# Kernel tuning notes

Hardware: AMD Instinct MI355X
Metric: run time of the kernel (lower is better)

## Reference

```python
import jax, jax.numpy as jnp
import numpy as np

NUM_RELATIONS = 3
NUM_HEADS = 1

N_NODES = 50000
N_EDGES = 300000
D = 256  # in_channels == out_channels == out_channels*num_heads
W_SCALE = 0.02  # realistic init scale; keeps linear-attention normalizer dominated by N_r


def setup_inputs() -> dict:
    key = jax.random.key(0)
    k = jax.random.split(key, 7)
    x = jax.random.normal(k[0], (N_NODES, D), dtype=jnp.float32)
    Wq = jax.random.normal(k[1], (NUM_RELATIONS, D, D * NUM_HEADS), dtype=jnp.float32) * W_SCALE
    Wk = jax.random.normal(k[2], (NUM_RELATIONS, D, D * NUM_HEADS), dtype=jnp.float32) * W_SCALE
    Wv = jax.random.normal(k[3], (NUM_RELATIONS, D, D * NUM_HEADS), dtype=jnp.float32) * W_SCALE
    Whp = jax.random.normal(k[4], (D * NUM_HEADS, D), dtype=jnp.float32) * W_SCALE
    edge_index = jax.random.randint(k[5], (2, N_EDGES), 0, N_NODES, dtype=jnp.int64)
    edge_type = jax.random.randint(k[6], (N_EDGES,), 0, NUM_RELATIONS, dtype=jnp.int64)
    return {"x": x, "Wq": Wq, "Wk": Wk, "Wv": Wv, "Whp": Whp,
            "edge_index": edge_index, "edge_type": edge_type}


def _trans_conv(x, Wq, Wk, Wv, Whp, edge_index, edge_type):
    # x: [N, F], Wq/Wk/Wv: [R, F, H*Dh], Whp: [H*Dh, Dh], edge_index: [2, E]
    row, col = edge_index[0], edge_index[1]
    N = x.shape[0]
    R = Wq.shape[0]
    H = NUM_HEADS
    Dh = Wq.shape[-1] // H
    xr = x[row]  # [E, F] gathered source-node features
    xc = x[col]  # [E, F] gathered target-node features
    x_out = jnp.zeros((N, Dh), dtype=x.dtype)
    for r in range(R):  # small fixed relation loop (structurally distinct weights)
        m = (edge_type == r).astype(x.dtype)  # [E] relation mask (handles ragged sizes)
        Nr = jnp.sum(m)  # number of edges of this relation (the 'N' in full_attention_conv)
        q = (xr @ Wq[r]).reshape(-1, H, Dh)  # [E, H, Dh]
        kk = (xc @ Wk[r]).reshape(-1, H, Dh)
        v = (xc @ Wv[r]).reshape(-1, H, Dh)
        # linear attention (no softmax), masked so only relation-r edges contribute
        kvs = jnp.einsum('e,ehm,ehd->hmd', m, kk, v)        # [H, Dh, Dh]
        num = jnp.einsum('ehm,hmd->ehd', q, kvs) + Nr * v    # [E, H, Dh]
        ks_sum = jnp.einsum('e,ehm->hm', m, kk)              # [H, Dh]
        norm = jnp.einsum('ehm,hm->eh', q, ks_sum)[..., None] + Nr  # [E, H, 1]
        attn = (num / norm).mean(axis=1)                     # [E, Dh] (mean over heads)
        x_out = x_out.at[row].add(m[:, None] * attn)         # scatter-add to source nodes
    return x_out @ Whp  # head projection


def reference(x, Wq, Wk, Wv, Whp, edge_index, edge_type):
    return _trans_conv(x, Wq, Wk, Wv, Whp, edge_index, edge_type)
```

## Files before the change

kernel.cpp:

```cpp
#include <hip/hip_runtime.h>

#define NN 50000
#define EE 300000
#define DD 256
#define RR 3
#define NPAD 50048
#define GS 64
#define SCT (RR * NN)
#define SCB 1024
#define SNB ((SCT + SCB - 1) / SCB)
#define TBLK 3128
#define WBLK 2560
#define CBLK 512
#define SBLK 12500

using bf16x8 = __attribute__((ext_vector_type(8))) short;
using f32x4  = __attribute__((ext_vector_type(4))) float;

__device__ __forceinline__ float bf2f(unsigned short u) {
    return __uint_as_float(((unsigned)u) << 16);
}
__device__ __forceinline__ unsigned short f2bf(float f) {
    unsigned u = __float_as_uint(f);
    return (unsigned short)((u + 0x7fffu + ((u >> 16) & 1u)) >> 16);
}
__device__ __forceinline__ void gload_lds16(const void* g, void* l) {
    __builtin_amdgcn_global_load_lds(
        (const __attribute__((address_space(1))) unsigned int*)g,
        (__attribute__((address_space(3))) unsigned int*)l, 16, 0, 0);
}

__global__ __launch_bounds__(256) void prep_tc(
    const float* __restrict__ x, const float* __restrict__ Wq,
    const float* __restrict__ Wk, const float* __restrict__ Wv,
    const float* __restrict__ Whp,
    unsigned short* __restrict__ xb, unsigned short* __restrict__ xT,
    unsigned short* __restrict__ Wqb, unsigned short* __restrict__ Wkb,
    unsigned short* __restrict__ Wvb, unsigned short* __restrict__ WhpT,
    const int* __restrict__ erow, const int* __restrict__ ecol,
    const int* __restrict__ etype, int* __restrict__ c_in,
    int* __restrict__ c_out, int* __restrict__ nr)
{
    const int tid = threadIdx.x;
    if (blockIdx.x < TBLK) {
        __shared__ unsigned short t[64][66];
        const int tb = blockIdx.x;
        const int n0 = (tb % 782) * 64, i0 = (tb / 782) * 64;
        const int nl = tid >> 2, c0 = (tid & 3) * 16;
        unsigned short vb[16];
        int n = n0 + nl;
        if (n < NN) {
            const float* src = x + (size_t)n * DD + i0 + c0;
#pragma unroll
            for (int q = 0; q < 16; q += 4) {
                float4 v = *(const float4*)(src + q);
                vb[q] = f2bf(v.x); vb[q + 1] = f2bf(v.y);
                vb[q + 2] = f2bf(v.z); vb[q + 3] = f2bf(v.w);
            }
#pragma unroll
            for (int q = 0; q < 16; q += 4)
                *(ushort4*)(xb + (size_t)n * DD + i0 + c0 + q) =
                    make_ushort4(vb[q], vb[q + 1], vb[q + 2], vb[q + 3]);
        } else {
#pragma unroll
            for (int q = 0; q < 16; q++) vb[q] = 0;
        }
#pragma unroll
        for (int q = 0; q < 16; q++) t[nl][c0 + q] = vb[q];
        __syncthreads();
        const int il = tid >> 2, nc0 = (tid & 3) * 16;
        unsigned short ob[16];
#pragma unroll
        for (int q = 0; q < 16; q++) ob[q] = t[nc0 + q][il];
#pragma unroll
        for (int q = 0; q < 16; q += 4)
            *(ushort4*)(xT + (size_t)(i0 + il) * NPAD + n0 + nc0 + q) =
                make_ushort4(ob[q], ob[q + 1], ob[q + 2], ob[q + 3]);
    } else if (blockIdx.x < TBLK + WBLK) {
        int t = (blockIdx.x - TBLK) * 256 + tid;
        int slot = t >> 16, o = t & 65535;
        int a = o >> 8, b = o & 255;
        if (slot < 3)       Wqb[(size_t)slot * 65536 + o] = f2bf(Wq[(size_t)slot * 65536 + o]);
        else if (slot < 6)  Wkb[(size_t)(slot - 3) * 65536 + o] = f2bf(Wk[(size_t)(slot - 3) * 65536 + o]);
        else if (slot < 9)  Wvb[(size_t)(slot - 6) * 65536 + o] = f2bf(Wv[(size_t)(slot - 6) * 65536 + o]);
        else if (slot == 9) WhpT[o] = f2bf(Whp[b * 256 + a]);
    } else {
        __shared__ int lnr[RR];
        if (tid < RR) lnr[tid] = 0;
        __syncthreads();
        int cb = blockIdx.x - (TBLK + WBLK);
        for (int e = cb * 256 + tid; e < EE; e += CBLK * 256) {
            int t = etype[e];
            atomicAdd(&c_out[t * NN + erow[e]], 1);
            atomicAdd(&c_in[t * NN + ecol[e]], 1);
            atomicAdd(&lnr[t], 1);
        }
        __syncthreads();
        if (tid < RR) atomicAdd(&nr[tid], lnr[tid]);
    }
}

__global__ __launch_bounds__(256) void prep2(
    const int* __restrict__ c_out, int* __restrict__ bsum,
    const unsigned short* __restrict__ xT, const int* __restrict__ c_in,
    float* __restrict__ xw, unsigned short* __restrict__ wbf)
{
    const int tid = threadIdx.x;
    if (blockIdx.x < SNB) {
        __shared__ int ws[4];
        const int b = blockIdx.x;
        const int i = b * SCB + tid * 4;
        int s = 0;
        if (i < SCT) {
            int4 v = *(const int4*)(c_out + i);
            s = v.x + v.y + v.z + v.w;
        }
#pragma unroll
        for (int off = 32; off; off >>= 1) s += __shfl_down(s, off, 64);
        if ((tid & 63) == 0) ws[tid >> 6] = s;
        __syncthreads();
        if (tid == 0) bsum[b] = ws[0] + ws[1] + ws[2] + ws[3];
    } else if (blockIdx.x < SNB + 256) {
        __shared__ float red[3][4];
        const int i = blockIdx.x - SNB;
        float a0 = 0.f, a1 = 0.f, a2 = 0.f;
        for (int n = tid * 4; n < NN; n += 1024) {
            ushort4 xv = *(const ushort4*)(xT + (size_t)i * NPAD + n);
            int4 w0 = *(const int4*)(c_in + n);
            int4 w1 = *(const int4*)(c_in + NN + n);
            int4 w2 = *(const int4*)(c_in + 2 * NN + n);
            float f0 = bf2f(xv.x), f1 = bf2f(xv.y), f2 = bf2f(xv.z), f3 = bf2f(xv.w);
            a0 += f0 * w0.x + f1 * w0.y + f2 * w0.z + f3 * w0.w;
            a1 += f0 * w1.x + f1 * w1.y + f2 * w1.z + f3 * w1.w;
            a2 += f0 * w2.x + f1 * w2.y + f2 * w2.z + f3 * w2.w;
        }
#pragma unroll
        for (int off = 32; off; off >>= 1) {
            a0 += __shfl_down(a0, off, 64);
            a1 += __shfl_down(a1, off, 64);
            a2 += __shfl_down(a2, off, 64);
        }
        if ((tid & 63) == 0) {
            red[0][tid >> 6] = a0; red[1][tid >> 6] = a1; red[2][tid >> 6] = a2;
        }
        __syncthreads();
        if (tid < 3)
            xw[tid * 256 + i] = red[tid][0] + red[tid][1] + red[tid][2] + red[tid][3];
    } else {
        int t = (blockIdx.x - SNB - 256) * 256 + tid;
        if (t < 3 * NPAD) {
            int r = t / NPAD, n = t % NPAD;
            wbf[t] = f2bf(n < NN ? (float)c_in[r * NN + n] : 0.f);
        }
    }
}

__global__ __launch_bounds__(256) void scan_bot(
    const int* __restrict__ cnt, const int* __restrict__ bsum,
    int* __restrict__ off, int* __restrict__ cur)
{
    __shared__ int bs[256], loc[256];
    const int b = blockIdx.x, tid = threadIdx.x;
    int v = tid < SNB ? bsum[tid] : 0;
    bs[tid] = v;
    __syncthreads();
    for (int d = 1; d < 256; d <<= 1) {
        int t = (tid >= d) ? bs[tid - d] : 0;
        __syncthreads();
        bs[tid] += t;
        __syncthreads();
    }
    const int myboff = b ? bs[b - 1] : 0;
    const int total = bs[255];
    const int i = b * SCB + tid * 4;
    int4 vv = make_int4(0, 0, 0, 0);
    if (i < SCT) vv = *(const int4*)(cnt + i);
    int s = vv.x + vv.y + vv.z + vv.w;
    loc[tid] = s;
    __syncthreads();
    for (int d = 1; d < 256; d <<= 1) {
        int t = (tid >= d) ? loc[tid - d] : 0;
        __syncthreads();
        loc[tid] += t;
        __syncthreads();
    }
    if (i < SCT) {
        int pre = myboff + (tid ? loc[tid - 1] : 0);
        int4 o;
        o.x = pre;
        o.y = pre + vv.x;
        o.z = pre + vv.x + vv.y;
        o.w = pre + vv.x + vv.y + vv.z;
        *(int4*)(off + i) = o;
        *(int4*)(cur + i) = o;
    }
    if (b == 0 && tid == 0) off[SCT] = total;
}

__global__ __launch_bounds__(256) void fill_kernel(
    const int* __restrict__ erow, const int* __restrict__ ecol,
    const int* __restrict__ etype, int* __restrict__ cur,
    int* __restrict__ scol)
{
    int e = blockIdx.x * 256 + threadIdx.x;
    if (e < EE) {
        int key = etype[e] * NN + erow[e];
        int p = atomicAdd(&cur[key], 1);
        scol[p] = ecol[e];
    }
}

__global__ __launch_bounds__(512) void g_kernel(
    const unsigned short* __restrict__ xT, const unsigned short* __restrict__ wbf,
    float* __restrict__ Gp)
{
    __shared__ __align__(16) char ldsA[16384];
    __shared__ __align__(16) char ldsB[16384];
    const int tid = threadIdx.x, lane = tid & 63, wid = tid >> 6;
    const int wr = wid >> 1, wc = wid & 1;
    const int i0 = blockIdx.x * 128, j0 = blockIdx.y * 128;
    const int TPZ = (NPAD / 64 + GS - 1) / GS;
    const int kt0 = blockIdx.z * TPZ;
    const int kt1 = min(NPAD / 64, kt0 + TPZ);

    f32x4 acc[3][2][4];
#pragma unroll
    for (int r = 0; r < 3; r++)
#pragma unroll
        for (int m = 0; m < 2; m++)
#pragma unroll
            for (int n = 0; n < 4; n++) acc[r][m][n] = (f32x4){0.f, 0.f, 0.f, 0.f};

    for (int kt = kt0; kt < kt1; kt++) {
        const int kbyte = kt * 128;
#pragma unroll
        for (int is = 0; is < 2; is++) {
            int lb = is * 8192 + wid * 1024;
            int d = lb + lane * 16;
            int row = d >> 7;
            int sc_ = (d & 127) ^ ((row & 7) << 4);
            gload_lds16((const char*)xT + (size_t)(i0 + row) * (NPAD * 2) + kbyte + sc_, ldsA + lb);
            gload_lds16((const char*)xT + (size_t)(j0 + row) * (NPAD * 2) + kbyte + sc_, ldsB + lb);
        }
        __syncthreads();
#pragma unroll
        for (int kk = 0; kk < 2; kk++) {
            const int cb = kk * 64 + ((lane >> 4) << 4);
            bf16x8 bfr[4];
#pragma unroll
            for (int n = 0; n < 4; n++) {
                int rn = wc * 64 + n * 16 + (lane & 15);
                bfr[n] = *(const bf16x8*)(ldsB + rn * 128 + (cb ^ ((rn & 7) << 4)));
            }
            float au[2][8];
#pragma unroll
            for (int m = 0; m < 2; m++) {
                int row = wr * 32 + m * 16 + (lane & 15);
                bf16x8 ar = *(const bf16x8*)(ldsA + row * 128 + (cb ^ ((row & 7) << 4)));
#pragma unroll
                for (int q = 0; q < 8; q++) au[m][q] = bf2f((unsigned short)ar[q]);
            }
            const int nb = kt * 64 + kk * 32 + ((lane >> 4) << 3);
#pragma unroll
            for (int r = 0; r < 3; r++) {
                bf16x8 wv = *(const bf16x8*)(wbf + (size_t)r * NPAD + nb);
                float wf[8];
#pragma unroll
                for (int q = 0; q < 8; q++) wf[q] = bf2f((unsigned short)wv[q]);
                bf16x8 am[2];
#pragma unroll
                for (int m = 0; m < 2; m++)
#pragma unroll
                    for (int q = 0; q < 8; q++)
                        am[m][q] = (short)f2bf(au[m][q] * wf[q]);
#pragma unroll
                for (int m = 0; m < 2; m++)
#pragma unroll
                    for (int n = 0; n < 4; n++)
                        acc[r][m][n] = __builtin_amdgcn_mfma_f32_16x16x32_bf16(
                            am[m], bfr[n], acc[r][m][n], 0, 0, 0);
            }
        }
        __syncthreads();
    }
    float* base = Gp + ((size_t)blockIdx.z * 4 + blockIdx.x * 2 + blockIdx.y) * 3 * 16384;
#pragma unroll
    for (int r = 0; r < 3; r++)
#pragma unroll
        for (int m = 0; m < 2; m++)
#pragma unroll
            for (int n = 0; n < 4; n++) {
                int col = wc * 64 + n * 16 + (lane & 15);
                int rw0 = wr * 32 + m * 16 + ((lane >> 4) << 2);
#pragma unroll
                for (int reg = 0; reg < 4; reg++)
                    base[r * 16384 + (rw0 + reg) * 128 + col] = acc[r][m][n][reg];
            }
}

__global__ __launch_bounds__(256) void greduce_kernel(
    const float* __restrict__ Gp, unsigned short* __restrict__ Gb)
{
    int gid = blockIdx.x * 256 + threadIdx.x;
    int t = gid >> 14, rem = gid & 16383;
    int r = t % 3, tile = t / 3;
    float s = 0.f;
    for (int z = 0; z < GS; z++)
        s += Gp[(size_t)z * 196608 + ((size_t)tile * 3 + r) * 16384 + rem];
    int i = (tile >> 1) * 128 + (rem >> 7);
    int j = (tile & 1) * 128 + (rem & 127);
    Gb[(size_t)r * 65536 + i * 256 + j] = f2bf(s);
}

__global__ __launch_bounds__(256) void matvec_bf(
    const unsigned short* __restrict__ Mat, const float* __restrict__ v,
    float* __restrict__ y)
{
    __shared__ float vs[256];
    const int b = blockIdx.x;
    const int r = b >> 6, rb = (b & 63) * 4;
    const int tid = threadIdx.x;
    vs[tid] = v[r * 256 + tid];
    __syncthreads();
    const int wid = tid >> 6, lane = tid & 63;
    const int row = rb + wid;
    ushort4 m4 = *(const ushort4*)(Mat + (size_t)r * 65536 + row * 256 + lane * 4);
    float s = bf2f(m4.x) * vs[lane * 4] + bf2f(m4.y) * vs[lane * 4 + 1] +
              bf2f(m4.z) * vs[lane * 4 + 2] + bf2f(m4.w) * vs[lane * 4 + 3];
#pragma unroll
    for (int off = 32; off; off >>= 1) s += __shfl_down(s, off, 64);
    if (lane == 0) y[r * 256 + row] = s;
}

__global__ __launch_bounds__(256) void sssum_kernel(
    const unsigned short* __restrict__ xb, const int* __restrict__ scol,
    const int* __restrict__ off, const float* __restrict__ tv,
    const int* __restrict__ c_out, const int* __restrict__ nr,
    unsigned short* __restrict__ Sraw, float* __restrict__ s1g,
    float* __restrict__ s2g)
{
    const int tid = threadIdx.x;
    const int wid = tid >> 6, lane = tid & 63;
    if (blockIdx.x < SBLK) {
        __shared__ float ts[768];
        __shared__ float nrs[RR];
        for (int k = tid; k < 768; k += 256) ts[k] = tv[k];
        if (tid < RR) nrs[tid] = (float)nr[tid];
        __syncthreads();
        const int n = blockIdx.x * 4 + wid;
        if (n >= NN) return;
        ushort4 xv = *(const ushort4*)(xb + (size_t)n * DD + lane * 4);
        float xf[4] = {bf2f(xv.x), bf2f(xv.y), bf2f(xv.z), bf2f(xv.w)};
#pragma unroll
        for (int t = 0; t < RR; t++) {
            float s = xf[0] * ts[t * 256 + lane * 4] + xf[1] * ts[t * 256 + lane * 4 + 1] +
                      xf[2] * ts[t * 256 + lane * 4 + 2] + xf[3] * ts[t * 256 + lane * 4 + 3];
#pragma unroll
            for (int o = 32; o; o >>= 1) s += __shfl_xor(s, o, 64);
            if (lane == 0) {
                float nrf = nrs[t];
                float denom = s + nrf;
                int cnt = c_out[t * NN + n];
                s2g[(size_t)t * NN + n] = cnt ? (float)cnt / denom : 0.f;
                s1g[(size_t)t * NN + n] = nrf / denom;
            }
        }
    } else {
        int seg = (blockIdx.x - SBLK) * 4 + wid;
        if (seg >= SCT) return;
        int b0 = off[seg], b1 = off[seg + 1];
        float a0 = 0.f, a1 = 0.f, a2 = 0.f, a3 = 0.f;
        for (int i = b0; i < b1; i++) {
            int col = scol[i];
            ushort4 v = *(const ushort4*)(xb + (size_t)col * DD + lane * 4);
            a0 += bf2f(v.x); a1 += bf2f(v.y); a2 += bf2f(v.z); a3 += bf2f(v.w);
        }
        int t = seg / NN, n = seg - t * NN;
        ushort4 o;
        o.x = f2bf(a0); o.y = f2bf(a1); o.z = f2bf(a2); o.w = f2bf(a3);
        *(ushort4*)(Sraw + (size_t)n * 768 + t * 256 + lane * 4) = o;
    }
}

template <int MODE, int SWZ>
__global__ __launch_bounds__(256) void gemm_nt(
    const unsigned short* __restrict__ A, int lda,
    const unsigned short* __restrict__ B, int ldb,
    void* __restrict__ Cv, int ldc, int M, int KK,
    size_t sa, size_t sb, size_t sc)
{
    A += (size_t)blockIdx.z * sa;
    B += (size_t)blockIdx.z * sb;
    __shared__ __align__(16) char ldsA[16384];
    __shared__ __align__(16) char ldsB[16384];
    const int tid = threadIdx.x, lane = tid & 63, wid = tid >> 6;
    const int wr = wid >> 1, wc = wid & 1;
    int bx = blockIdx.x;
    if (SWZ) {
        int nwg = gridDim.x, q = nwg >> 3, rem = nwg & 7;
        int xcd = bx & 7, idx = bx >> 3;
        bx = (xcd < rem ? xcd * (q + 1) : rem * (q + 1) + (xcd - rem) * q) + idx;
    }
    const int row0 = bx * 128, col0 = blockIdx.y * 128;

    f32x4 acc[4][4];
#pragma unroll
    for (int m = 0; m < 4; m++)
#pragma unroll
        for (int n = 0; n < 4; n++) acc[m][n] = (f32x4){0.f, 0.f, 0.f, 0.f};

    for (int k0 = 0; k0 < KK; k0 += 64) {
#pragma unroll
        for (int is = 0; is < 4; is++) {
            int lb = is * 4096 + wid * 1024;
            int d = lb + lane * 16;
            int row = d >> 7;
            int sc_ = (d & 127) ^ ((row & 7) << 4);
            int gr = row0 + row; gr = gr < M ? gr : M - 1;
            gload_lds16((const char*)(A + (size_t)gr * lda + k0) + sc_, ldsA + lb);
            int rn = col0 + row;
            gload_lds16((const char*)(B + (size_t)rn * ldb + k0) + sc_, ldsB + lb);
        }
        __syncthreads();
#pragma unroll
        for (int kk = 0; kk < 2; kk++) {
            bf16x8 af[4], bf_[4];
            const int cb = kk * 64 + ((lane >> 4) << 4);
#pragma unroll
            for (int m = 0; m < 4; m++) {
                int row = wr * 64 + m * 16 + (lane & 15);
                af[m] = *(const bf16x8*)(ldsA + row * 128 + (cb ^ ((row & 7) << 4)));
                int rn = wc * 64 + m * 16 + (lane & 15);
                bf_[m] = *(const bf16x8*)(ldsB + rn * 128 + (cb ^ ((rn & 7) << 4)));
            }
#pragma unroll
            for (int m = 0; m < 4; m++)
#pragma unroll
                for (int n = 0; n < 4; n++)
                    acc[m][n] = __builtin_amdgcn_mfma_f32_16x16x32_bf16(
                        af[m], bf_[n], acc[m][n], 0, 0, 0);
        }
        __syncthreads();
    }

#pragma unroll
    for (int m = 0; m < 4; m++) {
#pragma unroll
        for (int reg = 0; reg < 4; reg++) {
            int r = row0 + wr * 64 + m * 16 + ((lane >> 4) << 2) + reg;
            if (r >= M) continue;
#pragma unroll
            for (int n = 0; n < 4; n++) {
                int c = col0 + wc * 64 + n * 16 + (lane & 15);
                float v = acc[m][n][reg];
                if (MODE == 0)
                    ((unsigned short*)Cv)[(size_t)blockIdx.z * sc + (size_t)r * ldc + c] = f2bf(v);
                else
                    ((float*)Cv)[(size_t)blockIdx.z * sc + (size_t)r * ldc + c] = v;
            }
        }
    }
}

__global__ __launch_bounds__(512) void gemm_big(
    const unsigned short* __restrict__ Xb, const unsigned short* __restrict__ Sraw,
    const unsigned short* __restrict__ Bm, const float* __restrict__ s2g,
    const float* __restrict__ s1g, float* __restrict__ C, int M)
{
    extern __shared__ __align__(16) char lds[];
    char* ldsA = lds;
    char* ldsB = lds + 32768;
    float* sl  = (float*)(lds + 98304);
    const int tid = threadIdx.x, lane = tid & 63, wid = tid >> 6;
    const int wr = wid >> 2, wc = wid & 3;
    int bx = blockIdx.x;
    {
        int nwg = gridDim.x, q = nwg >> 3, rem = nwg & 7;
        int xcd = bx & 7, idx = bx >> 3;
        bx = (xcd < rem ? xcd * (q + 1) : rem * (q + 1) + (xcd - rem) * q) + idx;
    }
    const int row0 = bx * 128;

    for (int k = tid; k < 768; k += 512) {
        int pp = k >> 7, rr = k & 127;
        int gr = row0 + rr; gr = gr < M ? gr : M - 1;
        sl[k] = pp < 3 ? s2g[(size_t)pp * NN + gr] : s1g[(size_t)(pp - 3) * NN + gr];
    }

    f32x4 accO[4][4], acc[4][4];
#pragma unroll
    for (int m = 0; m < 4; m++)
#pragma unroll
        for (int n = 0; n < 4; n++) {
            accO[m][n] = (f32x4){0.f, 0.f, 0.f, 0.f};
            acc[m][n]  = (f32x4){0.f, 0.f, 0.f, 0.f};
        }

#define STAGE_A(buf, Asrc, ldaE, kE)                                           \
    { _Pragma("unroll")                                                        \
      for (int is = 0; is < 2; is++) {                                         \
          int lb = is * 8192 + wid * 1024;                                     \
          int d = lb + lane * 16;                                              \
          int row = d >> 7;                                                    \
          int sc_ = (d & 127) ^ ((row & 7) << 4);                              \
          int gr = row0 + row; gr = gr < M ? gr : M - 1;                       \
          gload_lds16((const char*)((Asrc) + (size_t)gr * (ldaE) + (kE)) + sc_,\
                      ldsA + (buf) * 16384 + lb); } }

#define STAGE_B(buf, kE)                                                       \
    { _Pragma("unroll")                                                        \
      for (int is = 0; is < 4; is++) {                                         \
          int lb = is * 8192 + wid * 1024;                                     \
          int d = lb + lane * 16;                                              \
          int row = d >> 7;                                                    \
          int sc_ = (d & 127) ^ ((row & 7) << 4);                              \
          gload_lds16((const char*)(Bm + (size_t)row * 1536 + (kE)) + sc_,     \
                      ldsB + (buf) * 32768 + lb); } }

#define MFMA_STEP(abuf, bbuf, ACC)                                             \
    { const char* bA = ldsA + (abuf) * 16384;                                  \
      const char* bB = ldsB + (bbuf) * 32768;                                  \
      _Pragma("unroll")                                                        \
      for (int kk = 0; kk < 2; kk++) {                                         \
          bf16x8 af[4], bf_[4];                                                \
          const int cb = kk * 64 + ((lane >> 4) << 4);                         \
          _Pragma("unroll")                                                    \
          for (int m = 0; m < 4; m++) {                                        \
              int row = wr * 64 + m * 16 + (lane & 15);                        \
              af[m] = *(const bf16x8*)(bA + row * 128 + (cb ^ ((row & 7) << 4)));\
              int rn = wc * 64 + m * 16 + (lane & 15);                         \
              bf_[m] = *(const bf16x8*)(bB + rn * 128 + (cb ^ ((rn & 7) << 4)));\
          }                                                                    \
          _Pragma("unroll")                                                    \
          for (int m = 0; m < 4; m++)                                          \
              _Pragma("unroll")                                                \
              for (int n = 0; n < 4; n++)                                      \
                  ACC[m][n] = __builtin_amdgcn_mfma_f32_16x16x32_bf16(         \
                      af[m], bf_[n], ACC[m][n], 0, 0, 0); } }

    STAGE_A(0, Xb, 256, 0);
    STAGE_B(0, 0);
    __syncthreads();
    int ab = 0, bb = 0;

    for (int st = 0; st < 24; st++) {
        if (st < 23) {
            int nst = st + 1;
            if (nst < 12) { STAGE_A(ab ^ 1, Xb, 256, (nst & 3) * 64); }
            else          { STAGE_A(ab ^ 1, Sraw, 768, (nst - 12) * 64); }
            STAGE_B(bb ^ 1, nst * 64);
        }
        MFMA_STEP(ab, bb, acc);
        __syncthreads();
        ab ^= 1; bb ^= 1;
        if ((st & 3) == 3) {
            int pp = st >> 2;
#pragma unroll
            for (int m = 0; m < 4; m++) {
                f32x4 sv = *(const f32x4*)&sl[pp * 128 + wr * 64 + m * 16 + ((lane >> 4) << 2)];
#pragma unroll
                for (int n = 0; n < 4; n++) {
                    accO[m][n] += sv * acc[m][n];
                    acc[m][n] = (f32x4){0.f, 0.f, 0.f, 0.f};
                }
            }
        }
    }
#undef STAGE_A
#undef STAGE_B
#undef MFMA_STEP

#pragma unroll
    for (int m = 0; m < 4; m++) {
#pragma unroll
        for (int reg = 0; reg < 4; reg++) {
            int r = row0 + wr * 64 + m * 16 + ((lane >> 4) << 2) + reg;
            if (r >= M) continue;
#pragma unroll
            for (int n = 0; n < 4; n++) {
                int c = wc * 64 + n * 16 + (lane & 15);
                C[(size_t)r * 256 + c] = accO[m][n][reg];
            }
        }
    }
}

extern "C" void kernel_launch(void* const* d_in, const int* in_sizes, int n_in,
                              void* d_out, int out_size, void* d_ws, size_t ws_size,
                              hipStream_t stream)
{
    const float* x   = (const float*)d_in[0];
    const float* Wq  = (const float*)d_in[1];
    const float* Wk  = (const float*)d_in[2];
    const float* Wv  = (const float*)d_in[3];
    const float* Whp = (const float*)d_in[4];
    const int* eidx  = (const int*)d_in[5];
    const int* etyp  = (const int*)d_in[6];
    const int* erow = eidx;
    const int* ecol = eidx + EE;
    float* out = (float*)d_out;

    char* p = (char*)d_ws;
    unsigned short* xb    = (unsigned short*)p; p += (size_t)NN * DD * 2;
    unsigned short* xT    = (unsigned short*)p; p += (size_t)DD * NPAD * 2;
    char*           regB  = p;                  p += (size_t)NN * 768 * 2;
    unsigned short* Gb    = (unsigned short*)p; p += (size_t)RR * 65536 * 2;
    unsigned short* M1    = (unsigned short*)p; p += (size_t)RR * 65536 * 2;
    unsigned short* Tm    = (unsigned short*)p; p += (size_t)RR * 65536 * 2;
    unsigned short* Bout  = (unsigned short*)p; p += (size_t)256 * 1536 * 2;
    unsigned short* Wqb   = (unsigned short*)p; p += (size_t)RR * 65536 * 2;
    unsigned short* Wkb   = (unsigned short*)p; p += (size_t)RR * 65536 * 2;
    unsigned short* Wvb   = (unsigned short*)p; p += (size_t)RR * 65536 * 2;
    unsigned short* WhpT  = (unsigned short*)p; p += 65536 * 2;
    unsigned short* wbf   = (unsigned short*)p; p += (size_t)RR * NPAD * 2;
    float*          xw    = (float*)p;          p += 768 * 4;
    float*          tv    = (float*)p;          p += 768 * 4;
    float*          s2g   = (float*)p;          p += (size_t)RR * NN * 4;
    float*          s1g   = (float*)p;          p += (size_t)RR * NN * 4;
    int*            c_in  = (int*)p;            p += (size_t)RR * NN * 4;
    int*            c_out = (int*)p;            p += (size_t)RR * NN * 4;
    int*            nr    = (int*)p;            p += 4 * 4;
    int*            off   = (int*)p;            p += (size_t)(RR * NN + 4) * 4;
    int*            cur   = (int*)p;            p += (size_t)RR * NN * 4;
    int*            scol  = (int*)p;            p += (size_t)EE * 4;
    int*            bsum  = (int*)p;            p += SNB * 4;
    float*          Gp    = (float*)regB;
    unsigned short* Sraw  = (unsigned short*)regB;

    hipFuncSetAttribute((const void*)gemm_big,
                        hipFuncAttributeMaxDynamicSharedMemorySize, 101376);

    hipMemsetAsync(c_in, 0, (size_t)(6 * NN + 4) * sizeof(int), stream);
    prep_tc<<<TBLK + WBLK + CBLK, 256, 0, stream>>>(
        x, Wq, Wk, Wv, Whp, xb, xT, Wqb, Wkb, Wvb, WhpT,
        erow, ecol, etyp, c_in, c_out, nr);
    prep2<<<SNB + 256 + (3 * NPAD + 255) / 256, 256, 0, stream>>>(
        c_out, bsum, xT, c_in, xw, wbf);
    scan_bot<<<SNB, 256, 0, stream>>>(c_out, bsum, off, cur);
    fill_kernel<<<(EE + 255) / 256, 256, 0, stream>>>(erow, ecol, etyp, cur, scol);

    gemm_nt<0, 0><<<dim3(2, 2, 3), 256, 0, stream>>>(Wqb, 256, Wkb, 256, M1, 256, 256, 256,
                                                     65536, 65536, 65536);
    gemm_nt<0, 0><<<dim3(2, 2, 3), 256, 0, stream>>>(WhpT, 256, Wvb, 256, Bout + 768, 1536,
                                                     256, 256, 0, 65536, 256);

    g_kernel<<<dim3(2, 2, GS), 512, 0, stream>>>(xT, wbf, Gp);
    greduce_kernel<<<12 * 64, 256, 0, stream>>>(Gp, Gb);

    gemm_nt<0, 0><<<dim3(2, 2, 3), 256, 0, stream>>>(M1, 256, Gb, 256, Tm, 256, 256, 256,
                                                     65536, 65536, 65536);
    gemm_nt<0, 0><<<dim3(2, 2, 3), 256, 0, stream>>>(Bout + 768, 1536, Tm, 256, Bout, 1536,
                                                     256, 256, 256, 65536, 256);
    matvec_bf<<<192, 256, 0, stream>>>(M1, xw, tv);

    sssum_kernel<<<SBLK + (SCT + 3) / 4, 256, 0, stream>>>(
        xb, scol, off, tv, c_out, nr, Sraw, s1g, s2g);

    const int MB2 = (NN + 127) / 128;
    gemm_big<<<dim3(MB2, 1), 512, 101376, stream>>>(xb, Sraw, Bout, s2g, s1g, out, NN);
}
```

Baseline: 310.3 us.

## Fuse Gram-matrix kernel with scaled neighbor-sum pass and prescale scatter operand

Merges the partial Gram-matrix MFMA kernel and the per-node normalizer/neighbor-sum kernel into one launch, so the 256 GEMM blocks run alongside the gather blocks instead of leaving most of the GPU idle. To allow this, the matvec that produces tv moves earlier, and Gp gets its own workspace region instead of aliasing the scatter buffer. The neighbor sums are now scaled by s1 before the bf16 store, so gemm_big no longer needs s1 scaling and its last 12 k-steps accumulate straight into the output accumulator. The cost is a larger workspace, a heavier fused kernel whose GEMM blocks use lots of registers and LDS, and bf16 rounding applied after the s1 scaling.

Measured after the change: 418.2 us. +34.8%, slower.

```diff
diff --git a/kernel.cpp b/kernel.cpp
--- a/kernel.cpp
+++ b/kernel.cpp
@@ -12,7 +12,7 @@
 #define TBLK 3128
 #define WBLK 2560
 #define CBLK 512
-#define SBLK 12500
+#define GBLK 256
 
 using bf16x8 = __attribute__((ext_vector_type(8))) short;
 using f32x4  = __attribute__((ext_vector_type(4))) float;
@@ -210,92 +210,141 @@
     }
 }
 
-__global__ __launch_bounds__(512) void g_kernel(
+__global__ __launch_bounds__(512) void gg_kernel(
     const unsigned short* __restrict__ xT, const unsigned short* __restrict__ wbf,
-    float* __restrict__ Gp)
+    float* __restrict__ Gp,
+    const unsigned short* __restrict__ xb, const int* __restrict__ scol,
+    const int* __restrict__ off, const float* __restrict__ tv,
+    const int* __restrict__ c_out, const int* __restrict__ nr,
+    unsigned short* __restrict__ Ascat, float* __restrict__ s2g)
 {
     __shared__ __align__(16) char ldsA[16384];
     __shared__ __align__(16) char ldsB[16384];
+    __shared__ float ts[768];
+    __shared__ float nrs[RR];
     const int tid = threadIdx.x, lane = tid & 63, wid = tid >> 6;
-    const int wr = wid >> 1, wc = wid & 1;
-    const int i0 = blockIdx.x * 128, j0 = blockIdx.y * 128;
-    const int TPZ = (NPAD / 64 + GS - 1) / GS;
-    const int kt0 = blockIdx.z * TPZ;
-    const int kt1 = min(NPAD / 64, kt0 + TPZ);
-
-    f32x4 acc[3][2][4];
-#pragma unroll
-    for (int r = 0; r < 3; r++)
-#pragma unroll
-        for (int m = 0; m < 2; m++)
-#pragma unroll
-            for (int n = 0; n < 4; n++) acc[r][m][n] = (f32x4){0.f, 0.f, 0.f, 0.f};
-
-    for (int kt = kt0; kt < kt1; kt++) {
-        const int kbyte = kt * 128;
-#pragma unroll
-        for (int is = 0; is < 2; is++) {
-            int lb = is * 8192 + wid * 1024;
-            int d = lb + lane * 16;
-            int row = d >> 7;
-            int sc_ = (d & 127) ^ ((row & 7) << 4);
-            gload_lds16((const char*)xT + (size_t)(i0 + row) * (NPAD * 2) + kbyte + sc_, ldsA + lb);
-            gload_lds16((const char*)xT + (size_t)(j0 + row) * (NPAD * 2) + kbyte + sc_, ldsB + lb);
-        }
-        __syncthreads();
-#pragma unroll
-        for (int kk = 0; kk < 2; kk++) {
-            const int cb = kk * 64 + ((lane >> 4) << 4);
-            bf16x8 bfr[4];
-#pragma unroll
-            for (int n = 0; n < 4; n++) {
-                int rn = wc * 64 + n * 16 + (lane & 15);
-                bfr[n] = *(const bf16x8*)(ldsB + rn * 128 + (cb ^ ((rn & 7) << 4)));
-            }
-            float au[2][8];
-#pragma unroll
-            for (int m = 0; m < 2; m++) {
-                int row = wr * 32 + m * 16 + (lane & 15);
-                bf16x8 ar = *(const bf16x8*)(ldsA + row * 128 + (cb ^ ((row & 7) << 4)));
-#pragma unroll
-                for (int q = 0; q < 8; q++) au[m][q] = bf2f((unsigned short)ar[q]);
-            }
-            const int nb = kt * 64 + kk * 32 + ((lane >> 4) << 3);
-#pragma unroll
-            for (int r = 0; r < 3; r++) {
-                bf16x8 wv = *(const bf16x8*)(wbf + (size_t)r * NPAD + nb);
-                float wf[8];
-#pragma unroll
-                for (int q = 0; q < 8; q++) wf[q] = bf2f((unsigned short)wv[q]);
-                bf16x8 am[2];
-#pragma unroll
-                for (int m = 0; m < 2; m++)
-#pragma unroll
-                    for (int q = 0; q < 8; q++)
-                        am[m][q] = (short)f2bf(au[m][q] * wf[q]);
-#pragma unroll
-                for (int m = 0; m < 2; m++)
-#pragma unroll
-                    for (int n = 0; n < 4; n++)
-                        acc[r][m][n] = __builtin_amdgcn_mfma_f32_16x16x32_bf16(
-                            am[m], bfr[n], acc[r][m][n], 0, 0, 0);
-            }
-        }
-        __syncthreads();
-    }
-    float* base = Gp + ((size_t)blockIdx.z * 4 + blockIdx.x * 2 + blockIdx.y) * 3 * 16384;
-#pragma unroll
-    for (int r = 0; r < 3; r++)
-#pragma unroll
-        for (int m = 0; m < 2; m++)
-#pragma unroll
-            for (int n = 0; n < 4; n++) {
-                int col = wc * 64 + n * 16 + (lane & 15);
-                int rw0 = wr * 32 + m * 16 + ((lane >> 4) << 2);
-#pragma unroll
-                for (int reg = 0; reg < 4; reg++)
-                    base[r * 16384 + (rw0 + reg) * 128 + col] = acc[r][m][n][reg];
-            }
+
+    if (blockIdx.x < GBLK) {
+        const int gz = blockIdx.x & 63, gj = (blockIdx.x >> 6) & 1, gi = blockIdx.x >> 7;
+        const int wr = wid >> 1, wc = wid & 1;
+        const int i0 = gi * 128, j0 = gj * 128;
+        const int TPZ = (NPAD / 64 + GS - 1) / GS;
+        const int kt0 = gz * TPZ;
+        const int kt1 = min(NPAD / 64, kt0 + TPZ);
+
+        f32x4 acc[3][2][4];
+#pragma unroll
+        for (int r = 0; r < 3; r++)
+#pragma unroll
+            for (int m = 0; m < 2; m++)
+#pragma unroll
+                for (int n = 0; n < 4; n++) acc[r][m][n] = (f32x4){0.f, 0.f, 0.f, 0.f};
+
+        for (int kt = kt0; kt < kt1; kt++) {
+            const int kbyte = kt * 128;
+#pragma unroll
+            for (int is = 0; is < 2; is++) {
+                int lb = is * 8192 + wid * 1024;
+                int d = lb + lane * 16;
+                int row = d >> 7;
+                int sc_ = (d & 127) ^ ((row & 7) << 4);
+                gload_lds16((const char*)xT + (size_t)(i0 + row) * (NPAD * 2) + kbyte + sc_, ldsA + lb);
+                gload_lds16((const char*)xT + (size_t)(j0 + row) * (NPAD * 2) + kbyte + sc_, ldsB + lb);
+            }
+            __syncthreads();
+#pragma unroll
+            for (int kk = 0; kk < 2; kk++) {
+                const int cb = kk * 64 + ((lane >> 4) << 4);
+                bf16x8 bfr[4];
+#pragma unroll
+                for (int n = 0; n < 4; n++) {
+                    int rn = wc * 64 + n * 16 + (lane & 15);
+                    bfr[n] = *(const bf16x8*)(ldsB + rn * 128 + (cb ^ ((rn & 7) << 4)));
+                }
+                float au[2][8];
+#pragma unroll
+                for (int m = 0; m < 2; m++) {
+                    int row = wr * 32 + m * 16 + (lane & 15);
+                    bf16x8 ar = *(const bf16x8*)(ldsA + row * 128 + (cb ^ ((row & 7) << 4)));
+#pragma unroll
+                    for (int q = 0; q < 8; q++) au[m][q] = bf2f((unsigned short)ar[q]);
+                }
+                const int nb = kt * 64 + kk * 32 + ((lane >> 4) << 3);
+#pragma unroll
+                for (int r = 0; r < 3; r++) {
+                    bf16x8 wv = *(const bf16x8*)(wbf + (size_t)r * NPAD + nb);
+                    float wf[8];
+#pragma unroll
+                    for (int q = 0; q < 8; q++) wf[q] = bf2f((unsigned short)wv[q]);
+                    bf16x8 am[2];
+#pragma unroll
+                    for (int m = 0; m < 2; m++)
+#pragma unroll
+                        for (int q = 0; q < 8; q++)
+                            am[m][q] = (short)f2bf(au[m][q] * wf[q]);
+#pragma unroll
+                    for (int m = 0; m < 2; m++)
+#pragma unroll
+                        for (int n = 0; n < 4; n++)
+                            acc[r][m][n] = __builtin_amdgcn_mfma_f32_16x16x32_bf16(
+                                am[m], bfr[n], acc[r][m][n], 0, 0, 0);
+                }
+            }
+            __syncthreads();
+        }
+        float* base = Gp + ((size_t)gz * 4 + gi * 2 + gj) * 3 * 16384;
+#pragma unroll
+        for (int r = 0; r < 3; r++)
+#pragma unroll
+            for (int m = 0; m < 2; m++)
+#pragma unroll
+                for (int n = 0; n < 4; n++) {
+                    int col = wc * 64 + n * 16 + (lane & 15);
+                    int rw0 = wr * 32 + m * 16 + ((lane >> 4) << 2);
+#pragma unroll
+                    for (int reg = 0; reg < 4; reg++)
+                        base[r * 16384 + (rw0 + reg) * 128 + col] = acc[r][m][n][reg];
+                }
+    } else {
+        for (int k = tid; k < 768; k += 512) ts[k] = tv[k];
+        if (tid < RR) nrs[tid] = (float)nr[tid];
+        __syncthreads();
+        const int n = (blockIdx.x - GBLK) * 8 + wid;
+        if (n >= NN) return;
+        ushort4 xv = *(const ushort4*)(xb + (size_t)n * DD + lane * 4);
+        float xf[4] = {bf2f(xv.x), bf2f(xv.y), bf2f(xv.z), bf2f(xv.w)};
+        float dots[RR];
+#pragma unroll
+        for (int t = 0; t < RR; t++) {
+            float s = xf[0] * ts[t * 256 + lane * 4] + xf[1] * ts[t * 256 + lane * 4 + 1] +
+                      xf[2] * ts[t * 256 + lane * 4 + 2] + xf[3] * ts[t * 256 + lane * 4 + 3];
+#pragma unroll
+            for (int o = 32; o; o >>= 1) s += __shfl_xor(s, o, 64);
+            dots[t] = s;
+        }
+#pragma unroll
+        for (int t = 0; t < RR; t++) {
+            float nrf = nrs[t];
+            float denom = dots[t] + nrf;
+            if (lane == 0) {
+                int cnt = c_out[t * NN + n];
+                s2g[(size_t)t * NN + n] = cnt ? (float)cnt / denom : 0.f;
+            }
+            float acc[4] = {0.f, 0.f, 0.f, 0.f};
+            int b0 = off[t * NN + n], b1 = off[t * NN + n + 1];
+            for (int i = b0; i < b1; i++) {
+                int col = scol[i];
+                ushort4 v = *(const ushort4*)(xb + (size_t)col * DD + lane * 4);
+                acc[0] += bf2f(v.x); acc[1] += bf2f(v.y);
+                acc[2] += bf2f(v.z); acc[3] += bf2f(v.w);
+            }
+            float s1 = nrf / denom;
+            ushort4 o2;
+            o2.x = f2bf(s1 * acc[0]); o2.y = f2bf(s1 * acc[1]);
+            o2.z = f2bf(s1 * acc[2]); o2.w = f2bf(s1 * acc[3]);
+            *(ushort4*)(Ascat + (size_t)n * 768 + t * 256 + lane * 4) = o2;
+        }
+    }
 }
 
 __global__ __launch_bounds__(256) void greduce_kernel(
@@ -332,56 +381,6 @@
     if (lane == 0) y[r * 256 + row] = s;
 }
 
-__global__ __launch_bounds__(256) void sssum_kernel(
-    const unsigned short* __restrict__ xb, const int* __restrict__ scol,
-    const int* __restrict__ off, const float* __restrict__ tv,
-    const int* __restrict__ c_out, const int* __restrict__ nr,
-    unsigned short* __restrict__ Sraw, float* __restrict__ s1g,
-    float* __restrict__ s2g)
-{
-    const int tid = threadIdx.x;
-    const int wid = tid >> 6, lane = tid & 63;
-    if (blockIdx.x < SBLK) {
-        __shared__ float ts[768];
-        __shared__ float nrs[RR];
-        for (int k = tid; k < 768; k += 256) ts[k] = tv[k];
-        if (tid < RR) nrs[tid] = (float)nr[tid];
-        __syncthreads();
-        const int n = blockIdx.x * 4 + wid;
-        if (n >= NN) return;
-        ushort4 xv = *(const ushort4*)(xb + (size_t)n * DD + lane * 4);
-        float xf[4] = {bf2f(xv.x), bf2f(xv.y), bf2f(xv.z), bf2f(xv.w)};
-#pragma unroll
-        for (int t = 0; t < RR; t++) {
-            float s = xf[0] * ts[t * 256 + lane * 4] + xf[1] * ts[t * 256 + lane * 4 + 1] +
-                      xf[2] * ts[t * 256 + lane * 4 + 2] + xf[3] * ts[t * 256 + lane * 4 + 3];
-#pragma unroll
-            for (int o = 32; o; o >>= 1) s += __shfl_xor(s, o, 64);
-            if (lane == 0) {
-                float nrf = nrs[t];
-                float denom = s + nrf;
-                int cnt = c_out[t * NN + n];
-                s2g[(size_t)t * NN + n] = cnt ? (float)cnt / denom : 0.f;
-                s1g[(size_t)t * NN + n] = nrf / denom;
-            }
-        }
-    } else {
-        int seg = (blockIdx.x - SBLK) * 4 + wid;
-        if (seg >= SCT) return;
-        int b0 = off[seg], b1 = off[seg + 1];
-        float a0 = 0.f, a1 = 0.f, a2 = 0.f, a3 = 0.f;
-        for (int i = b0; i < b1; i++) {
-            int col = scol[i];
-            ushort4 v = *(const ushort4*)(xb + (size_t)col * DD + lane * 4);
-            a0 += bf2f(v.x); a1 += bf2f(v.y); a2 += bf2f(v.z); a3 += bf2f(v.w);
-        }
-        int t = seg / NN, n = seg - t * NN;
-        ushort4 o;
-        o.x = f2bf(a0); o.y = f2bf(a1); o.z = f2bf(a2); o.w = f2bf(a3);
-        *(ushort4*)(Sraw + (size_t)n * 768 + t * 256 + lane * 4) = o;
-    }
-}
-
 template <int MODE, int SWZ>
 __global__ __launch_bounds__(256) void gemm_nt(
     const unsigned short* __restrict__ A, int lda,
@@ -463,14 +462,14 @@
 }
 
 __global__ __launch_bounds__(512) void gemm_big(
-    const unsigned short* __restrict__ Xb, const unsigned short* __restrict__ Sraw,
+    const unsigned short* __restrict__ Xb, const unsigned short* __restrict__ As,
     const unsigned short* __restrict__ Bm, const float* __restrict__ s2g,
-    const float* __restrict__ s1g, float* __restrict__ C, int M)
+    float* __restrict__ C, int M)
 {
     extern __shared__ __align__(16) char lds[];
     char* ldsA = lds;
     char* ldsB = lds + 32768;
-    float* sl  = (float*)(lds + 98304);
+    float* s2l = (float*)(lds + 98304);
     const int tid = threadIdx.x, lane = tid & 63, wid = tid >> 6;
     const int wr = wid >> 2, wc = wid & 3;
     int bx = blockIdx.x;
@@ -481,10 +480,10 @@
     }
     const int row0 = bx * 128;
 
-    for (int k = tid; k < 768; k += 512) {
-        int pp = k >> 7, rr = k & 127;
+    if (tid < 384) {
+        int rsel = tid >> 7, rr = tid & 127;
         int gr = row0 + rr; gr = gr < M ? gr : M - 1;
-        sl[k] = pp < 3 ? s2g[(size_t)pp * NN + gr] : s1g[(size_t)(pp - 3) * NN + gr];
+        s2l[tid] = s2g[(size_t)rsel * NN + gr];
     }
 
     f32x4 accO[4][4], acc[4][4];
@@ -543,28 +542,34 @@
     __syncthreads();
     int ab = 0, bb = 0;
 
-    for (int st = 0; st < 24; st++) {
-        if (st < 23) {
-            int nst = st + 1;
-            if (nst < 12) { STAGE_A(ab ^ 1, Xb, 256, (nst & 3) * 64); }
-            else          { STAGE_A(ab ^ 1, Sraw, 768, (nst - 12) * 64); }
-            STAGE_B(bb ^ 1, nst * 64);
-        }
-        MFMA_STEP(ab, bb, acc);
+    for (int r = 0; r < 3; r++) {
+        for (int kt = 0; kt < 4; kt++) {
+            if (kt < 3)      { STAGE_A(ab ^ 1, Xb, 256, (kt + 1) * 64);
+                               STAGE_B(bb ^ 1, r * 256 + (kt + 1) * 64); }
+            else if (r < 2)  { STAGE_A(ab ^ 1, Xb, 256, 0);
+                               STAGE_B(bb ^ 1, (r + 1) * 256); }
+            else             { STAGE_A(ab ^ 1, As, 768, 0);
+                               STAGE_B(bb ^ 1, 768); }
+            MFMA_STEP(ab, bb, acc);
+            __syncthreads();
+            ab ^= 1; bb ^= 1;
+        }
+#pragma unroll
+        for (int m = 0; m < 4; m++) {
+            f32x4 sv = *(const f32x4*)&s2l[r * 128 + wr * 64 + m * 16 + ((lane >> 4) << 2)];
+#pragma unroll
+            for (int n = 0; n < 4; n++) {
+                accO[m][n] += sv * acc[m][n];
+                acc[m][n] = (f32x4){0.f, 0.f, 0.f, 0.f};
+            }
+        }
+    }
+    for (int st = 0; st < 12; st++) {
+        if (st < 11) { STAGE_A(ab ^ 1, As, 768, (st + 1) * 64);
+                       STAGE_B(bb ^ 1, 768 + (st + 1) * 64); }
+        MFMA_STEP(ab, bb, accO);
         __syncthreads();
         ab ^= 1; bb ^= 1;
-        if ((st & 3) == 3) {
-            int pp = st >> 2;
-#pragma unroll
-            for (int m = 0; m < 4; m++) {
-                f32x4 sv = *(const f32x4*)&sl[pp * 128 + wr * 64 + m * 16 + ((lane >> 4) << 2)];
-#pragma unroll
-                for (int n = 0; n < 4; n++) {
-                    accO[m][n] += sv * acc[m][n];
-                    acc[m][n] = (f32x4){0.f, 0.f, 0.f, 0.f};
-                }
-            }
-        }
     }
 #undef STAGE_A
 #undef STAGE_B
@@ -603,7 +608,8 @@
     char* p = (char*)d_ws;
     unsigned short* xb    = (unsigned short*)p; p += (size_t)NN * DD * 2;
     unsigned short* xT    = (unsigned short*)p; p += (size_t)DD * NPAD * 2;
-    char*           regB  = p;                  p += (size_t)NN * 768 * 2;
+    unsigned short* Ascat = (unsigned short*)p; p += (size_t)NN * 768 * 2;
+    float*          Gp    = (float*)p;          p += (size_t)GS * 196608 * 4;
     unsigned short* Gb    = (unsigned short*)p; p += (size_t)RR * 65536 * 2;
     unsigned short* M1    = (unsigned short*)p; p += (size_t)RR * 65536 * 2;
     unsigned short* Tm    = (unsigned short*)p; p += (size_t)RR * 65536 * 2;
@@ -616,7 +622,6 @@
     float*          xw    = (float*)p;          p += 768 * 4;
     float*          tv    = (float*)p;          p += 768 * 4;
     float*          s2g   = (float*)p;          p += (size_t)RR * NN * 4;
-    float*          s1g   = (float*)p;          p += (size_t)RR * NN * 4;
     int*            c_in  = (int*)p;            p += (size_t)RR * NN * 4;
     int*            c_out = (int*)p;            p += (size_t)RR * NN * 4;
     int*            nr    = (int*)p;            p += 4 * 4;
@@ -624,11 +629,9 @@
     int*            cur   = (int*)p;            p += (size_t)RR * NN * 4;
     int*            scol  = (int*)p;            p += (size_t)EE * 4;
     int*            bsum  = (int*)p;            p += SNB * 4;
-    float*          Gp    = (float*)regB;
-    unsigned short* Sraw  = (unsigned short*)regB;
 
     hipFuncSetAttribute((const void*)gemm_big,
-                        hipFuncAttributeMaxDynamicSharedMemorySize, 101376);
+                        hipFuncAttributeMaxDynamicSharedMemorySize, 99840);
 
     hipMemsetAsync(c_in, 0, (size_t)(6 * NN + 4) * sizeof(int), stream);
     prep_tc<<<TBLK + WBLK + CBLK, 256, 0, stream>>>(
@@ -643,19 +646,17 @@
                                                      65536, 65536, 65536);
     gemm_nt<0, 0><<<dim3(2, 2, 3), 256, 0, stream>>>(WhpT, 256, Wvb, 256, Bout + 768, 1536,
                                                      256, 256, 0, 65536, 256);
-
-    g_kernel<<<dim3(2, 2, GS), 512, 0, stream>>>(xT, wbf, Gp);
+    matvec_bf<<<192, 256, 0, stream>>>(M1, xw, tv);
+
+    gg_kernel<<<GBLK + (NN + 7) / 8, 512, 0, stream>>>(
+        xT, wbf, Gp, xb, scol, off, tv, c_out, nr, Ascat, s2g);
     greduce_kernel<<<12 * 64, 256, 0, stream>>>(Gp, Gb);
 
     gemm_nt<0, 0><<<dim3(2, 2, 3), 256, 0, stream>>>(M1, 256, Gb, 256, Tm, 256, 256, 256,
                                                      65536, 65536, 65536);
     gemm_nt<0, 0><<<dim3(2, 2, 3), 256, 0, stream>>>(Bout + 768, 1536, Tm, 256, Bout, 1536,
                                                      256, 256, 256, 65536, 256);
-    matvec_bf<<<192, 256, 0, stream>>>(M1, xw, tv);
-
-    sssum_kernel<<<SBLK + (SCT + 3) / 4, 256, 0, stream>>>(
-        xb, scol, off, tv, c_out, nr, Sraw, s1g, s2g);
 
     const int MB2 = (NN + 127) / 128;
-    gemm_big<<<dim3(MB2, 1), 512, 101376, stream>>>(xb, Sraw, Bout, s2g, s1g, out, NN);
-}
+    gemm_big<<<dim3(MB2, 1), 512, 99840, stream>>>(xb, Ascat, Bout, s2g, out, NN);
+}
```
